# Optimization experiments

Hardware: AMD Instinct MI355X
Metric: run time of the kernel (lower is better)

## Reference

```python
import jax, jax.numpy as jnp
import numpy as np
import math

B, S, D, H = 32, 197, 1024, 16  # batch, seq_len (pinned by w_o=Linear(197,.)), d_model, n_heads
DK = D // H                      # d_k = 64


def setup_inputs() -> dict:
    key = jax.random.key(0)
    ks = jax.random.split(key, 8)
    f32 = jnp.float32
    # weights scaled by 0.02 for numerically sane softmax logits
    return {
        "x0": jax.random.normal(ks[0], (B, S, D), dtype=f32),
        "x1": jax.random.normal(ks[1], (B, S, D), dtype=f32),
        "wk0": jax.random.normal(ks[2], (D, D), dtype=f32) * 0.02,
        "bk0": jnp.zeros((D,), dtype=f32),
        "wk1": jax.random.normal(ks[3], (D, D), dtype=f32) * 0.02,
        "bk1": jnp.zeros((D,), dtype=f32),
        "wv0": jax.random.normal(ks[4], (D, D), dtype=f32) * 0.02,
        "bv0": jnp.zeros((D,), dtype=f32),
        "wv1": jax.random.normal(ks[5], (D, D), dtype=f32) * 0.02,
        "bv1": jnp.zeros((D,), dtype=f32),
        "wo": jax.random.normal(ks[6], (D, S), dtype=f32) * 0.02,  # nn.Linear(197, d_model) weight: [d_model, 197]
        "bo": jnp.zeros((D,), dtype=f32),
    }


def _proj(x, w, b):
    # torch nn.Linear: y = x @ W^T + b; then view + transpose -> [B, H, S, DK]
    y = x @ w.T + b
    return y.reshape(B, S, H, DK).transpose(0, 2, 1, 3)


def reference(x0, x1, wk0, bk0, wk1, bk1, wv0, bv0, wv1, bv1, wo, bo):
    scale = 1.0 / math.sqrt(DK)
    K0 = _proj(x0, wk0, bk0)
    K1 = _proj(x1, wk1, bk1)
    V0 = _proj(x0, wv0, bv0)
    V1 = _proj(x1, wv1, bv1)
    # mutual attention: K_i @ K_j^T * scale for i != j  -> [B, H, S, S]
    s01 = jnp.einsum('bhsd,bhtd->bhst', K0, K1) * scale
    s10 = jnp.einsum('bhsd,bhtd->bhst', K1, K0) * scale
    a0 = jax.nn.softmax(s01, axis=-1)
    a1 = jax.nn.softmax(s10, axis=-1)
    # feature outputs: attn_i @ V_i  -> [B, H, S, DK]
    f0 = jnp.einsum('bhst,bhtd->bhsd', a0, V0)
    f1 = jnp.einsum('bhst,bhtd->bhsd', a1, V1)
    # cross-product combination, averaged over the 2 ordered pairs -> [B, H, S, S]
    comb = (jnp.einsum('bhsd,bhtd->bhst', f0, f1)
            + jnp.einsum('bhsd,bhtd->bhst', f1, f0)) * (scale * 0.5)
    # w_o: Linear(197 -> d_model) on last axis -> [B, H, S, D]
    out = comb @ wo.T + bo
    return (out, a0, a1)
```

## Files before the change

### kernel.cpp

```cpp
#include <hip/hip_runtime.h>
#include <hip/hip_bf16.h>

typedef unsigned short u16;
typedef __attribute__((ext_vector_type(8))) short short8;
typedef __attribute__((ext_vector_type(4))) float floatx4;
typedef __attribute__((ext_vector_type(4), aligned(4))) float floatx4u;
typedef __attribute__((ext_vector_type(4))) unsigned int uint4v;

#define B_ 32
#define S_ 197
#define D_ 1024
#define H_ 16
#define DK_ 64
#define BH_ 512
#define SP_ 208
#define TP_ 224
#define M_ 6304
#define XSZ_ ((size_t)M_*D_)
#define WSZ_W ((size_t)D_*D_)

#define KSZ ((size_t)BH_*SP_*DK_)
#define VSZ ((size_t)BH_*DK_*TP_)
#define CSZ ((size_t)BH_*SP_*TP_)
#define K0_OFF  ((size_t)0)
#define K1_OFF  (KSZ)
#define VT0_OFF (2*KSZ)
#define VT1_OFF (2*KSZ + VSZ)
#define F0_OFF  (2*KSZ + 2*VSZ)
#define F1_OFF  (3*KSZ + 2*VSZ)
#define COMB_OFF (4*KSZ + 2*VSZ)
#define WOT_OFF  (4*KSZ + 2*VSZ + CSZ)
#define BIAS_OFF (WOT_OFF + (size_t)D_*TP_)
#define WS_ELEMS (BIAS_OFF + 5*1024)

#define XB_OFF  (COMB_OFF)
#define WB_OFF  (COMB_OFF + 2*XSZ_)

#define OUT_SZ ((size_t)BH_*S_*D_)
#define A_SZ   ((size_t)BH_*S_*S_)

__device__ __forceinline__ float bf2f(u16 v) {
    unsigned u = ((unsigned)v) << 16;
    return __builtin_bit_cast(float, u);
}
__device__ __forceinline__ u16 f2bf(float f) {
    unsigned u = __builtin_bit_cast(unsigned, f);
    u += 0x7FFFu + ((u >> 16) & 1u);
    return (u16)(u >> 16);
}
__device__ __forceinline__ floatx4 mfma16(short8 a, short8 b, floatx4 c) {
    return __builtin_amdgcn_mfma_f32_16x16x32_bf16(a, b, c, 0, 0, 0);
}
__device__ __forceinline__ void gl_lds16(const u16* g, u16* l) {
    __builtin_amdgcn_global_load_lds(
        (const __attribute__((address_space(1))) void*)(g),
        (__attribute__((address_space(3))) void*)(l), 16, 0, 0);
}

__device__ __forceinline__ int detect_f32(const u16* __restrict__ x0raw) {
    int lane = threadIdx.x & 63;
    unsigned h = x0raw[2*lane];
    unsigned e = (h >> 7) & 0xFFu;
    int ext = (e < 0x30u) | (e > 0x4Fu);
    unsigned long long m = __ballot(ext);
    return __popcll(m) > 16;
}

__device__ __forceinline__ u16 loadBF(const void* p, size_t off, int is32) {
    return is32 ? f2bf(((const float*)p)[off]) : ((const u16*)p)[off];
}
__device__ __forceinline__ void storeF(void* p, size_t off, float v, int is32) {
    if (is32) ((float*)p)[off] = v; else ((u16*)p)[off] = f2bf(v);
}
__device__ __forceinline__ short8 load8(const void* p, size_t off, int is32) {
    short8 r;
    if (is32) {
        const float* f = (const float*)p + off;
        floatx4 a = *(const floatx4*)f;
        floatx4 b = *(const floatx4*)(f + 4);
        r[0]=(short)f2bf(a[0]); r[1]=(short)f2bf(a[1]);
        r[2]=(short)f2bf(a[2]); r[3]=(short)f2bf(a[3]);
        r[4]=(short)f2bf(b[0]); r[5]=(short)f2bf(b[1]);
        r[6]=(short)f2bf(b[2]); r[7]=(short)f2bf(b[3]);
    } else {
        r = *(const short8*)((const u16*)p + off);
    }
    return r;
}

__global__ __launch_bounds__(256) void prep_kernel(
    const void* __restrict__ wo,
    const void* __restrict__ bk0, const void* __restrict__ bk1,
    const void* __restrict__ bv0, const void* __restrict__ bv1,
    const void* __restrict__ bo,
    const void* __restrict__ x0, const void* __restrict__ x1,
    const void* __restrict__ wk0, const void* __restrict__ wk1,
    const void* __restrict__ wv0, const void* __restrict__ wv1,
    u16* __restrict__ ws) {
    int is32 = detect_f32((const u16*)x0);
    int i = blockIdx.x * 256 + threadIdx.x;
    if (i < D_*TP_) {
        int d = i / TP_, t = i - d*TP_;
        ws[WOT_OFF + i] = (t < S_) ? loadBF(wo, (size_t)d*S_ + t, is32) : (u16)0;
    }
    const int KP = BH_*(SP_-S_)*DK_;
    if (i < KP) {
        int bh = i / ((SP_-S_)*DK_);
        int r  = i - bh*((SP_-S_)*DK_);
        int s  = S_ + r / DK_;
        int dk = r % DK_;
        size_t o = ((size_t)bh*SP_ + s)*DK_ + dk;
        ws[K0_OFF + o] = 0; ws[K1_OFF + o] = 0;
    }
    const int VP = BH_*DK_*(TP_-S_);
    if (i < VP) {
        int bh = i / (DK_*(TP_-S_));
        int r  = i - bh*(DK_*(TP_-S_));
        int dk = r / (TP_-S_);
        int t  = S_ + r % (TP_-S_);
        size_t o = ((size_t)bh*DK_ + dk)*TP_ + t;
        ws[VT0_OFF + o] = 0; ws[VT1_OFF + o] = 0;
    }
    if (i < 5*1024) {
        int which = i >> 10, j = i & 1023;
        const void* src = (which==0) ? bk0 : (which==1) ? bk1
                        : (which==2) ? bv0 : (which==3) ? bv1 : bo;
        ws[BIAS_OFF + i] = loadBF(src, j, is32);
    }
    const size_t NCH = (2*XSZ_ + 4*WSZ_W) / 8;
    for (size_t c = (size_t)blockIdx.x*256 + threadIdx.x; c < NCH;
         c += (size_t)gridDim.x*256) {
        size_t e = c * 8;
        const void* src; size_t soff;
        if (e < 2*XSZ_) {
            src = (e < XSZ_) ? x0 : x1;
            soff = (e < XSZ_) ? e : e - XSZ_;
        } else {
            size_t r = e - 2*XSZ_;
            int z = (int)(r >> 20);
            src = (z==0) ? wk0 : (z==1) ? wk1 : (z==2) ? wv0 : wv1;
            soff = r & (WSZ_W - 1);
        }
        *(short8*)&ws[XB_OFF + e] = load8(src, soff, is32);
    }
}

__global__ __launch_bounds__(256) void proj_kernel(u16* __restrict__ ws)
{
    __shared__ __align__(16) u16 lA[128*64];
    __shared__ __align__(16) u16 lB[128*64];
    int z = blockIdx.z;
    const u16* X = ws + XB_OFF + (size_t)(z & 1)*XSZ_;
    const u16* W = ws + WB_OFF + (size_t)z*WSZ_W;
    u16* dst = ws + ((z==0) ? K0_OFF : (z==1) ? K1_OFF : (z==2) ? VT0_OFF : VT1_OFF);
    int m0 = blockIdx.x * 128, n0 = blockIdx.y * 128;
    int tid = threadIdx.x;
    int w = tid >> 6, lane = tid & 63, q = lane >> 4, l15 = lane & 15;
    int wm = (w >> 1) * 64, wn = (w & 1) * 64;

    floatx4 acc[4][4];
    #pragma unroll
    for (int a = 0; a < 4; a++)
        #pragma unroll
        for (int b = 0; b < 4; b++) acc[a][b] = (floatx4){0.f,0.f,0.f,0.f};

    for (int kk = 0; kk < D_; kk += 64) {
        __syncthreads();
        #pragma unroll
        for (int it = 0; it < 4; it++) {
            int c = it*256 + w*64 + lane;
            int r = c >> 3, cc = c & 7;
            int m = m0 + r; if (m > M_-1) m = M_-1;
            gl_lds16(X + (size_t)m*D_ + kk + cc*8,        &lA[(it*256 + w*64)*8]);
            gl_lds16(W + (size_t)(n0 + r)*D_ + kk + cc*8, &lB[(it*256 + w*64)*8]);
        }
        __syncthreads();
        #pragma unroll
        for (int kc = 0; kc < 2; kc++) {
            short8 af[4], bf[4];
            #pragma unroll
            for (int mi = 0; mi < 4; mi++)
                af[mi] = *(const short8*)&lA[(wm + mi*16 + l15)*64 + kc*32 + q*8];
            #pragma unroll
            for (int ni = 0; ni < 4; ni++)
                bf[ni] = *(const short8*)&lB[(wn + ni*16 + l15)*64 + kc*32 + q*8];
            #pragma unroll
            for (int mi = 0; mi < 4; mi++)
                #pragma unroll
                for (int ni = 0; ni < 4; ni++)
                    acc[mi][ni] = mfma16(af[mi], bf[ni], acc[mi][ni]);
        }
    }
    #pragma unroll
    for (int ni = 0; ni < 4; ni++) {
        int n = n0 + wn + ni*16 + l15;
        float bv = bf2f(ws[BIAS_OFF + (size_t)z*1024 + n]);
        int h = n >> 6, dk = n & 63;
        #pragma unroll
        for (int mi = 0; mi < 4; mi++)
            #pragma unroll
            for (int r = 0; r < 4; r++) {
                int m = m0 + wm + mi*16 + q*4 + r;
                if (m < M_) {
                    int b = m / S_;
                    int s = m - b * S_;
                    int bh = b * H_ + h;
                    size_t o = (z < 2) ? (((size_t)bh*SP_ + s)*DK_ + dk)
                                       : (((size_t)bh*DK_ + dk)*TP_ + s);
                    dst[o] = f2bf(acc[mi][ni][r] + bv);
                }
            }
    }
}

__global__ __launch_bounds__(256) void attn_kernel(const u16* __restrict__ ws,
                                                   void* __restrict__ dout,
                                                   const u16* __restrict__ x0det) {
    __shared__ __align__(16) u16 lKa[SP_*DK_];
    __shared__ __align__(16) u16 lKb[SP_*DK_];
    int is32 = detect_f32(x0det);
    int bh = blockIdx.x, dir = blockIdx.y;
    const u16* Ka = ws + (dir ? K1_OFF : K0_OFF) + (size_t)bh*SP_*DK_;
    const u16* Kb = ws + (dir ? K0_OFF : K1_OFF) + (size_t)bh*SP_*DK_;
    size_t aBase = OUT_SZ + (size_t)dir*A_SZ + (size_t)bh*S_*S_;
    int tid = threadIdx.x;
    for (int i = tid; i < SP_*DK_/8; i += 256) {
        ((uint4v*)lKa)[i] = ((const uint4v*)Ka)[i];
        ((uint4v*)lKb)[i] = ((const uint4v*)Kb)[i];
    }
    __syncthreads();
    int w = tid>>6, lane = tid&63, q = lane>>4, l15 = lane&15;
    const float scale = 0.125f;
    for (int rt = w; rt < 13; rt += 4) {
        floatx4 acc[13];
        #pragma unroll
        for (int ct = 0; ct < 13; ct++) acc[ct] = (floatx4){0.f,0.f,0.f,0.f};
        #pragma unroll
        for (int kc = 0; kc < 2; kc++) {
            short8 af = *(const short8*)&lKa[(rt*16 + l15)*DK_ + kc*32 + q*8];
            #pragma unroll
            for (int ct = 0; ct < 13; ct++) {
                short8 bf = *(const short8*)&lKb[(ct*16 + l15)*DK_ + kc*32 + q*8];
                acc[ct] = mfma16(af, bf, acc[ct]);
            }
        }
        #pragma unroll
        for (int r = 0; r < 4; r++) {
            int srow = rt*16 + q*4 + r;
            float v[13];
            float mx = -1e9f;
            #pragma unroll
            for (int ct = 0; ct < 13; ct++) {
                int t = ct*16 + l15;
                v[ct] = (t < S_) ? acc[ct][r]*scale : -1e9f;
                mx = fmaxf(mx, v[ct]);
            }
            #pragma unroll
            for (int off = 1; off < 16; off <<= 1) mx = fmaxf(mx, __shfl_xor(mx, off));
            float sum = 0.f;
            #pragma unroll
            for (int ct = 0; ct < 13; ct++) {
                int t = ct*16 + l15;
                float e = (t < S_) ? __expf(v[ct] - mx) : 0.f;
                v[ct] = e; sum += e;
            }
            #pragma unroll
            for (int off = 1; off < 16; off <<= 1) sum += __shfl_xor(sum, off);
            float inv = 1.0f / sum;
            if (srow < S_) {
                #pragma unroll
                for (int ct = 0; ct < 13; ct++) {
                    int t = ct*16 + l15;
                    if (t < S_) storeF(dout, aBase + (size_t)srow*S_ + t, v[ct]*inv, is32);
                }
            }
        }
    }
}

__global__ __launch_bounds__(256) void av_kernel(const void* __restrict__ dout,
                                                 u16* __restrict__ ws,
                                                 const u16* __restrict__ x0det) {
    __shared__ __align__(16) u16 lV[DK_*TP_];
    int is32 = detect_f32(x0det);
    int bh = blockIdx.x, dir = blockIdx.y;
    const u16* Vt = ws + (dir ? VT1_OFF : VT0_OFF) + (size_t)bh*DK_*TP_;
    size_t aBase = OUT_SZ + (size_t)dir*A_SZ + (size_t)bh*S_*S_;
    u16* fO = ws + (dir ? F1_OFF : F0_OFF) + (size_t)bh*SP_*DK_;
    int tid = threadIdx.x;
    for (int i = tid; i < DK_*TP_/8; i += 256)
        ((uint4v*)lV)[i] = ((const uint4v*)Vt)[i];
    __syncthreads();
    int w = tid>>6, lane = tid&63, q = lane>>4, l15 = lane&15;
    for (int rt = w; rt < 13; rt += 4) {
        int s = rt*16 + l15;
        bool sok = s < S_;
        size_t arow = aBase + (size_t)s*S_;
        floatx4 acc[4];
        #pragma unroll
        for (int ct = 0; ct < 4; ct++) acc[ct] = (floatx4){0.f,0.f,0.f,0.f};
        for (int kc = 0; kc < 7; kc++) {
            int t0 = kc*32 + q*8;
            short8 af;
            if (sok && t0 + 8 <= S_) {
                if (is32) {
                    const float* fp = (const float*)dout + arow + t0;
                    floatx4u a = *(const floatx4u*)fp;
                    floatx4u b = *(const floatx4u*)(fp + 4);
                    af[0]=(short)f2bf(a[0]); af[1]=(short)f2bf(a[1]);
                    af[2]=(short)f2bf(a[2]); af[3]=(short)f2bf(a[3]);
                    af[4]=(short)f2bf(b[0]); af[5]=(short)f2bf(b[1]);
                    af[6]=(short)f2bf(b[2]); af[7]=(short)f2bf(b[3]);
                } else {
                    #pragma unroll
                    for (int j = 0; j < 8; j++)
                        af[j] = (short)((const u16*)dout)[arow + t0 + j];
                }
            } else {
                #pragma unroll
                for (int j = 0; j < 8; j++) {
                    int t = t0 + j;
                    af[j] = (sok && t < S_) ? (short)loadBF(dout, arow + t, is32) : (short)0;
                }
            }
            #pragma unroll
            for (int ct = 0; ct < 4; ct++) {
                short8 bf = *(const short8*)&lV[(ct*16 + l15)*TP_ + kc*32 + q*8];
                acc[ct] = mfma16(af, bf, acc[ct]);
            }
        }
        #pragma unroll
        for (int ct = 0; ct < 4; ct++)
            #pragma unroll
            for (int r = 0; r < 4; r++) {
                int so = rt*16 + q*4 + r;
                fO[(size_t)so*DK_ + ct*16 + l15] = f2bf(acc[ct][r]);
            }
    }
}

__global__ __launch_bounds__(256) void comb_kernel(u16* __restrict__ ws) {
    __shared__ __align__(16) u16 lf0[SP_*DK_];
    __shared__ __align__(16) u16 lf1[SP_*DK_];
    int bh = blockIdx.x;
    const u16* f0 = ws + F0_OFF + (size_t)bh*SP_*DK_;
    const u16* f1 = ws + F1_OFF + (size_t)bh*SP_*DK_;
    u16* cO = ws + COMB_OFF + (size_t)bh*SP_*TP_;
    int tid = threadIdx.x;
    for (int i = tid; i < SP_*DK_/8; i += 256) {
        ((uint4v*)lf0)[i] = ((const uint4v*)f0)[i];
        ((uint4v*)lf1)[i] = ((const uint4v*)f1)[i];
    }
    __syncthreads();
    int w = tid>>6, lane = tid&63, q = lane>>4, l15 = lane&15;
    const float cscale = 0.0625f;
    for (int rt = w; rt < 13; rt += 4) {
        short8 a0f[2], a1f[2];
        #pragma unroll
        for (int kc = 0; kc < 2; kc++) {
            a0f[kc] = *(const short8*)&lf0[(rt*16 + l15)*DK_ + kc*32 + q*8];
            a1f[kc] = *(const short8*)&lf1[(rt*16 + l15)*DK_ + kc*32 + q*8];
        }
        for (int nt = 0; nt < 13; nt++) {
            floatx4 acc = (floatx4){0.f,0.f,0.f,0.f};
            #pragma unroll
            for (int kc = 0; kc < 2; kc++) {
                short8 b1 = *(const short8*)&lf1[(nt*16 + l15)*DK_ + kc*32 + q*8];
                acc = mfma16(a0f[kc], b1, acc);
            }
            #pragma unroll
            for (int kc = 0; kc < 2; kc++) {
                short8 b0 = *(const short8*)&lf0[(nt*16 + l15)*DK_ + kc*32 + q*8];
                acc = mfma16(a1f[kc], b0, acc);
            }
            #pragma unroll
            for (int r = 0; r < 4; r++) {
                int srow = rt*16 + q*4 + r;
                cO[(size_t)srow*TP_ + nt*16 + l15] = f2bf(acc[r]*cscale);
            }
        }
        #pragma unroll
        for (int r = 0; r < 4; r++) {
            int srow = rt*16 + q*4 + r;
            cO[(size_t)srow*TP_ + 208 + l15] = 0;
        }
    }
}

__global__ __launch_bounds__(256) void out_kernel(const u16* __restrict__ ws,
                                                  void* __restrict__ dout,
                                                  const u16* __restrict__ x0det) {
    __shared__ __align__(16) u16 lw[128*TP_];
    int is32 = detect_f32(x0det);
    int bh = blockIdx.x, nb = blockIdx.y;
    const u16* wot = ws + WOT_OFF + (size_t)nb*128*TP_;
    const u16* cI  = ws + COMB_OFF + (size_t)bh*SP_*TP_;
    size_t oBase = (size_t)bh*S_*D_;
    int tid = threadIdx.x;
    for (int i = tid; i < 128*TP_/8; i += 256)
        ((uint4v*)lw)[i] = ((const uint4v*)wot)[i];
    __syncthreads();
    int w = tid>>6, lane = tid&63, q = lane>>4, l15 = lane&15;
    for (int mt = w; mt < 13; mt += 4) {
        floatx4 acc[8];
        #pragma unroll
        for (int nt = 0; nt < 8; nt++) acc[nt] = (floatx4){0.f,0.f,0.f,0.f};
        for (int kc = 0; kc < 7; kc++) {
            short8 af = *(const short8*)&cI[(size_t)(mt*16 + l15)*TP_ + kc*32 + q*8];
            #pragma unroll
            for (int nt = 0; nt < 8; nt++) {
                short8 bf = *(const short8*)&lw[(nt*16 + l15)*TP_ + kc*32 + q*8];
                acc[nt] = mfma16(af, bf, acc[nt]);
            }
        }
        #pragma unroll
        for (int nt = 0; nt < 8; nt++) {
            int d = nb*128 + nt*16 + l15;
            float bv = bf2f(ws[BIAS_OFF + 4*1024 + d]);
            #pragma unroll
            for (int r = 0; r < 4; r++) {
                int s = mt*16 + q*4 + r;
                if (s < S_) storeF(dout, oBase + (size_t)s*D_ + d, acc[nt][r] + bv, is32);
            }
        }
    }
}

extern "C" void kernel_launch(void* const* d_in, const int* in_sizes, int n_in,
                              void* d_out, int out_size, void* d_ws, size_t ws_size,
                              hipStream_t stream) {
    const void* x0  = d_in[0];
    const void* x1  = d_in[1];
    const void* wk0 = d_in[2];
    const void* bk0 = d_in[3];
    const void* wk1 = d_in[4];
    const void* bk1 = d_in[5];
    const void* wv0 = d_in[6];
    const void* bv0 = d_in[7];
    const void* wv1 = d_in[8];
    const void* bv1 = d_in[9];
    const void* wo  = d_in[10];
    const void* bo  = d_in[11];
    u16* ws = (u16*)d_ws;
    const u16* x0det = (const u16*)x0;

    if (ws_size < WS_ELEMS * sizeof(u16)) return;

    prep_kernel<<<3456, 256, 0, stream>>>(wo, bk0, bk1, bv0, bv1, bo,
                                          x0, x1, wk0, wk1, wv0, wv1, ws);
    proj_kernel<<<dim3(50, 8, 4), 256, 0, stream>>>(ws);
    attn_kernel<<<dim3(BH_, 2), 256, 0, stream>>>(ws, d_out, x0det);
    av_kernel<<<dim3(BH_, 2), 256, 0, stream>>>(d_out, ws, x0det);
    comb_kernel<<<BH_, 256, 0, stream>>>(ws);
    out_kernel<<<dim3(BH_, 8), 256, 0, stream>>>(ws, d_out, x0det);
}
```

Baseline: 1.083 ms.

## Fuse attention softmax with AV product and swizzle/pad shared memory layouts

Merges the attention-softmax kernel and the attention-times-V kernel into one. The softmax probabilities are staged as bf16 in a per-wave shared buffer and fed straight into the AV MFMA, so the attention matrix is no longer re-read from global memory. Ka is now read directly from global instead of being staged in LDS, which frees LDS for V and the probability tile. It also adds an XOR swizzle for the K, f0 and f1 tiles and pads the V and wo tiles (row stride 232) to reduce LDS bank conflicts. The trade-off is higher LDS use per block, which may lower occupancy.

```diff
diff --git a/kernel.cpp b/kernel.cpp
--- a/kernel.cpp
+++ b/kernel.cpp
@@ -15,6 +15,7 @@
 #define BH_ 512
 #define SP_ 208
 #define TP_ 224
+#define TPP_ 232
 #define M_ 6304
 #define XSZ_ ((size_t)M_*D_)
 #define WSZ_W ((size_t)D_*D_)
@@ -213,23 +214,29 @@
     }
 }
 
-__global__ __launch_bounds__(256) void attn_kernel(const u16* __restrict__ ws,
-                                                   void* __restrict__ dout,
-                                                   const u16* __restrict__ x0det) {
-    __shared__ __align__(16) u16 lKa[SP_*DK_];
+__global__ __launch_bounds__(256) void attn_av_kernel(u16* __restrict__ ws,
+                                                      void* __restrict__ dout,
+                                                      const u16* __restrict__ x0det) {
     __shared__ __align__(16) u16 lKb[SP_*DK_];
+    __shared__ __align__(16) u16 lV[DK_*TPP_];
+    __shared__ __align__(16) u16 lP[4][16*TPP_];
     int is32 = detect_f32(x0det);
     int bh = blockIdx.x, dir = blockIdx.y;
     const u16* Ka = ws + (dir ? K1_OFF : K0_OFF) + (size_t)bh*SP_*DK_;
     const u16* Kb = ws + (dir ? K0_OFF : K1_OFF) + (size_t)bh*SP_*DK_;
+    const u16* Vt = ws + (dir ? VT1_OFF : VT0_OFF) + (size_t)bh*DK_*TP_;
+    u16* fO = ws + (dir ? F1_OFF : F0_OFF) + (size_t)bh*SP_*DK_;
     size_t aBase = OUT_SZ + (size_t)dir*A_SZ + (size_t)bh*S_*S_;
     int tid = threadIdx.x;
-    for (int i = tid; i < SP_*DK_/8; i += 256) {
-        ((uint4v*)lKa)[i] = ((const uint4v*)Ka)[i];
-        ((uint4v*)lKb)[i] = ((const uint4v*)Kb)[i];
+    for (int i = tid; i < SP_*8; i += 256)
+        ((uint4v*)lKb)[(i & ~7) | ((i ^ (i >> 3)) & 7)] = ((const uint4v*)Kb)[i];
+    for (int i = tid; i < DK_*28; i += 256) {
+        int row = i / 28, c = i - row*28;
+        ((uint4v*)lV)[row*29 + c] = ((const uint4v*)Vt)[i];
     }
     __syncthreads();
     int w = tid>>6, lane = tid&63, q = lane>>4, l15 = lane&15;
+    u16* lPw = &lP[w][0];
     const float scale = 0.125f;
     for (int rt = w; rt < 13; rt += 4) {
         floatx4 acc[13];
@@ -237,10 +244,11 @@
         for (int ct = 0; ct < 13; ct++) acc[ct] = (floatx4){0.f,0.f,0.f,0.f};
         #pragma unroll
         for (int kc = 0; kc < 2; kc++) {
-            short8 af = *(const short8*)&lKa[(rt*16 + l15)*DK_ + kc*32 + q*8];
+            short8 af = *(const short8*)&Ka[(size_t)(rt*16 + l15)*DK_ + kc*32 + q*8];
             #pragma unroll
             for (int ct = 0; ct < 13; ct++) {
-                short8 bf = *(const short8*)&lKb[(ct*16 + l15)*DK_ + kc*32 + q*8];
+                short8 bf = *(const short8*)&lKb[(ct*16 + l15)*DK_ +
+                                                 ((kc*32 + q*8) ^ ((l15 & 7) << 3))];
                 acc[ct] = mfma16(af, bf, acc[ct]);
             }
         }
@@ -267,66 +275,25 @@
             #pragma unroll
             for (int off = 1; off < 16; off <<= 1) sum += __shfl_xor(sum, off);
             float inv = 1.0f / sum;
-            if (srow < S_) {
-                #pragma unroll
-                for (int ct = 0; ct < 13; ct++) {
-                    int t = ct*16 + l15;
-                    if (t < S_) storeF(dout, aBase + (size_t)srow*S_ + t, v[ct]*inv, is32);
-                }
-            }
-        }
-    }
-}
-
-__global__ __launch_bounds__(256) void av_kernel(const void* __restrict__ dout,
-                                                 u16* __restrict__ ws,
-                                                 const u16* __restrict__ x0det) {
-    __shared__ __align__(16) u16 lV[DK_*TP_];
-    int is32 = detect_f32(x0det);
-    int bh = blockIdx.x, dir = blockIdx.y;
-    const u16* Vt = ws + (dir ? VT1_OFF : VT0_OFF) + (size_t)bh*DK_*TP_;
-    size_t aBase = OUT_SZ + (size_t)dir*A_SZ + (size_t)bh*S_*S_;
-    u16* fO = ws + (dir ? F1_OFF : F0_OFF) + (size_t)bh*SP_*DK_;
-    int tid = threadIdx.x;
-    for (int i = tid; i < DK_*TP_/8; i += 256)
-        ((uint4v*)lV)[i] = ((const uint4v*)Vt)[i];
-    __syncthreads();
-    int w = tid>>6, lane = tid&63, q = lane>>4, l15 = lane&15;
-    for (int rt = w; rt < 13; rt += 4) {
-        int s = rt*16 + l15;
-        bool sok = s < S_;
-        size_t arow = aBase + (size_t)s*S_;
-        floatx4 acc[4];
-        #pragma unroll
-        for (int ct = 0; ct < 4; ct++) acc[ct] = (floatx4){0.f,0.f,0.f,0.f};
+            bool rok = srow < S_;
+            #pragma unroll
+            for (int ct = 0; ct < 13; ct++) {
+                int t = ct*16 + l15;
+                float pv = rok ? v[ct]*inv : 0.f;
+                lPw[(q*4 + r)*TPP_ + ct*16 + l15] = f2bf(pv);
+                if (rok && t < S_) storeF(dout, aBase + (size_t)srow*S_ + t, pv, is32);
+            }
+            lPw[(q*4 + r)*TPP_ + 208 + l15] = 0;
+        }
+        floatx4 facc[4];
+        #pragma unroll
+        for (int ct = 0; ct < 4; ct++) facc[ct] = (floatx4){0.f,0.f,0.f,0.f};
         for (int kc = 0; kc < 7; kc++) {
-            int t0 = kc*32 + q*8;
-            short8 af;
-            if (sok && t0 + 8 <= S_) {
-                if (is32) {
-                    const float* fp = (const float*)dout + arow + t0;
-                    floatx4u a = *(const floatx4u*)fp;
-                    floatx4u b = *(const floatx4u*)(fp + 4);
-                    af[0]=(short)f2bf(a[0]); af[1]=(short)f2bf(a[1]);
-                    af[2]=(short)f2bf(a[2]); af[3]=(short)f2bf(a[3]);
-                    af[4]=(short)f2bf(b[0]); af[5]=(short)f2bf(b[1]);
-                    af[6]=(short)f2bf(b[2]); af[7]=(short)f2bf(b[3]);
-                } else {
-                    #pragma unroll
-                    for (int j = 0; j < 8; j++)
-                        af[j] = (short)((const u16*)dout)[arow + t0 + j];
-                }
-            } else {
-                #pragma unroll
-                for (int j = 0; j < 8; j++) {
-                    int t = t0 + j;
-                    af[j] = (sok && t < S_) ? (short)loadBF(dout, arow + t, is32) : (short)0;
-                }
-            }
+            short8 paf = *(const short8*)&lPw[l15*TPP_ + kc*32 + q*8];
             #pragma unroll
             for (int ct = 0; ct < 4; ct++) {
-                short8 bf = *(const short8*)&lV[(ct*16 + l15)*TP_ + kc*32 + q*8];
-                acc[ct] = mfma16(af, bf, acc[ct]);
+                short8 bf = *(const short8*)&lV[(ct*16 + l15)*TPP_ + kc*32 + q*8];
+                facc[ct] = mfma16(paf, bf, facc[ct]);
             }
         }
         #pragma unroll
@@ -334,7 +301,7 @@
             #pragma unroll
             for (int r = 0; r < 4; r++) {
                 int so = rt*16 + q*4 + r;
-                fO[(size_t)so*DK_ + ct*16 + l15] = f2bf(acc[ct][r]);
+                fO[(size_t)so*DK_ + ct*16 + l15] = f2bf(facc[ct][r]);
             }
     }
 }
@@ -347,30 +314,33 @@
     const u16* f1 = ws + F1_OFF + (size_t)bh*SP_*DK_;
     u16* cO = ws + COMB_OFF + (size_t)bh*SP_*TP_;
     int tid = threadIdx.x;
-    for (int i = tid; i < SP_*DK_/8; i += 256) {
-        ((uint4v*)lf0)[i] = ((const uint4v*)f0)[i];
-        ((uint4v*)lf1)[i] = ((const uint4v*)f1)[i];
+    for (int i = tid; i < SP_*8; i += 256) {
+        int d = (i & ~7) | ((i ^ (i >> 3)) & 7);
+        ((uint4v*)lf0)[d] = ((const uint4v*)f0)[i];
+        ((uint4v*)lf1)[d] = ((const uint4v*)f1)[i];
     }
     __syncthreads();
     int w = tid>>6, lane = tid&63, q = lane>>4, l15 = lane&15;
+    int sw = (l15 & 7) << 3;
     const float cscale = 0.0625f;
     for (int rt = w; rt < 13; rt += 4) {
         short8 a0f[2], a1f[2];
         #pragma unroll
         for (int kc = 0; kc < 2; kc++) {
-            a0f[kc] = *(const short8*)&lf0[(rt*16 + l15)*DK_ + kc*32 + q*8];
-            a1f[kc] = *(const short8*)&lf1[(rt*16 + l15)*DK_ + kc*32 + q*8];
+            int eo = (kc*32 + q*8) ^ sw;
+            a0f[kc] = *(const short8*)&lf0[(rt*16 + l15)*DK_ + eo];
+            a1f[kc] = *(const short8*)&lf1[(rt*16 + l15)*DK_ + eo];
         }
         for (int nt = 0; nt < 13; nt++) {
             floatx4 acc = (floatx4){0.f,0.f,0.f,0.f};
             #pragma unroll
             for (int kc = 0; kc < 2; kc++) {
-                short8 b1 = *(const short8*)&lf1[(nt*16 + l15)*DK_ + kc*32 + q*8];
+                short8 b1 = *(const short8*)&lf1[(nt*16 + l15)*DK_ + ((kc*32 + q*8) ^ sw)];
                 acc = mfma16(a0f[kc], b1, acc);
             }
             #pragma unroll
             for (int kc = 0; kc < 2; kc++) {
-                short8 b0 = *(const short8*)&lf0[(nt*16 + l15)*DK_ + kc*32 + q*8];
+                short8 b0 = *(const short8*)&lf0[(nt*16 + l15)*DK_ + ((kc*32 + q*8) ^ sw)];
                 acc = mfma16(a1f[kc], b0, acc);
             }
             #pragma unroll
@@ -390,15 +360,17 @@
 __global__ __launch_bounds__(256) void out_kernel(const u16* __restrict__ ws,
                                                   void* __restrict__ dout,
                                                   const u16* __restrict__ x0det) {
-    __shared__ __align__(16) u16 lw[128*TP_];
+    __shared__ __align__(16) u16 lw[128*TPP_];
     int is32 = detect_f32(x0det);
     int bh = blockIdx.x, nb = blockIdx.y;
     const u16* wot = ws + WOT_OFF + (size_t)nb*128*TP_;
     const u16* cI  = ws + COMB_OFF + (size_t)bh*SP_*TP_;
     size_t oBase = (size_t)bh*S_*D_;
     int tid = threadIdx.x;
-    for (int i = tid; i < 128*TP_/8; i += 256)
-        ((uint4v*)lw)[i] = ((const uint4v*)wot)[i];
+    for (int i = tid; i < 128*28; i += 256) {
+        int row = i / 28, c = i - row*28;
+        ((uint4v*)lw)[row*29 + c] = ((const uint4v*)wot)[i];
+    }
     __syncthreads();
     int w = tid>>6, lane = tid&63, q = lane>>4, l15 = lane&15;
     for (int mt = w; mt < 13; mt += 4) {
@@ -409,7 +381,7 @@
             short8 af = *(const short8*)&cI[(size_t)(mt*16 + l15)*TP_ + kc*32 + q*8];
             #pragma unroll
             for (int nt = 0; nt < 8; nt++) {
-                short8 bf = *(const short8*)&lw[(nt*16 + l15)*TP_ + kc*32 + q*8];
+                short8 bf = *(const short8*)&lw[(nt*16 + l15)*TPP_ + kc*32 + q*8];
                 acc[nt] = mfma16(af, bf, acc[nt]);
             }
         }
@@ -449,8 +421,7 @@
     prep_kernel<<<3456, 256, 0, stream>>>(wo, bk0, bk1, bv0, bv1, bo,
                                           x0, x1, wk0, wk1, wv0, wv1, ws);
     proj_kernel<<<dim3(50, 8, 4), 256, 0, stream>>>(ws);
-    attn_kernel<<<dim3(BH_, 2), 256, 0, stream>>>(ws, d_out, x0det);
-    av_kernel<<<dim3(BH_, 2), 256, 0, stream>>>(d_out, ws, x0det);
+    attn_av_kernel<<<dim3(BH_, 2), 256, 0, stream>>>(ws, d_out, x0det);
     comb_kernel<<<BH_, 256, 0, stream>>>(ws);
     out_kernel<<<dim3(BH_, 8), 256, 0, stream>>>(ws, d_out, x0det);
 }
```

New measurement: 1.100 ms. Within noise of the previous version (+1.5%).
